# Optimization experiments

Hardware: AMD Instinct MI355X
Metric: run time of the kernel (lower is better)

## Reference

```python
import jax, jax.numpy as jnp
import numpy as np

T, B = 128, 4096
TB = T * B
NUM_ACTIONS, N_WORDS, EMB = 6, 16, 16
IMG_FEAT, LOC_DIM, HID = 16, 4, 128
IN_DIM = IMG_FEAT + LOC_DIM + EMB  # 36
GRID_SIZE = 5.0


def setup_inputs() -> dict:
    key = jax.random.key(0)
    ks = jax.random.split(key, 32)
    p = lambda i, shape, s=0.1: (jax.random.normal(ks[i], shape, dtype=jnp.float32) * s)
    inp = {
        'image': jax.random.uniform(ks[0], (TB, 1, 3, 3), dtype=jnp.float32) * 255.0,
        'location': jax.random.uniform(ks[1], (TB, 2), dtype=jnp.float32) * GRID_SIZE,
        'message': jax.random.randint(ks[2], (TB,), 0, N_WORDS, dtype=jnp.int32),
        'done': (jax.random.uniform(ks[3], (TB,)) < 0.05).astype(jnp.float32),
        'h0': p(4, (B, HID)),
        'c0': p(5, (B, HID)),
        # visual encoder 9->256->256->128->16
        'vw1': p(6, (256, 9)), 'vb1': p(7, (256,)),
        'vw2': p(8, (256, 256)), 'vb2': p(9, (256,)),
        'vw3': p(10, (128, 256)), 'vb3': p(11, (128,)),
        'vw4': p(12, (IMG_FEAT, 128)), 'vb4': p(13, (IMG_FEAT,)),
        # message encoder: embedding + linear
        'emb': p(14, (N_WORDS, EMB)),
        'mw': p(15, (EMB, EMB)), 'mb': p(16, (EMB,)),
        # location encoder 2->4
        'lw': p(17, (LOC_DIM, 2)), 'lb': p(18, (LOC_DIM,)),
        # LSTM (PyTorch layout: gates ordered i,f,g,o)
        'w_ih': p(19, (4 * HID, IN_DIM)), 'w_hh': p(20, (4 * HID, HID)),
        'b_ih': p(21, (4 * HID,)), 'b_hh': p(22, (4 * HID,)),
        # heads
        'aw': p(23, (NUM_ACTIONS, HID), 0.01), 'ab': jnp.zeros((NUM_ACTIONS,), jnp.float32),
        'cw': p(24, (1, HID), 1.0), 'cb': jnp.zeros((1,), jnp.float32),
        'msw': p(25, (N_WORDS, HID), 0.01), 'msb': jnp.zeros((N_WORDS,), jnp.float32),
    }
    return inp


def _encode(image, location, message, vw1, vb1, vw2, vb2, vw3, vb3, vw4, vb4,
            emb, mw, mb, lw, lb):
    img = image.reshape(image.shape[0], -1) / 255.0  # [TB, 9]
    h = jax.nn.relu(img @ vw1.T + vb1)
    h = jax.nn.relu(h @ vw2.T + vb2)
    h = jax.nn.relu(h @ vw3.T + vb3)
    img_feat = jax.nn.relu(h @ vw4.T + vb4)           # [TB, 16]
    loc_feat = (location / GRID_SIZE) @ lw.T + lb     # [TB, 4]
    msg_feat = jax.nn.relu(emb[message] @ mw.T + mb)  # [TB, 16]
    return jnp.concatenate([img_feat, loc_feat, msg_feat], axis=1)  # [TB, 36]


def _lstm_scan(x, done, h0, c0, w_ih, w_hh, b_ih, b_hh):
    # x: [T, B, IN], done: [T, B]
    def step(carry, inp):
        h, c = carry
        xt, dt = inp
        mask = (1.0 - dt)[:, None]
        h = h * mask
        c = c * mask
        gates = xt @ w_ih.T + b_ih + h @ w_hh.T + b_hh  # [B, 4H]
        i, f, g, o = jnp.split(gates, 4, axis=1)
        i = jax.nn.sigmoid(i); f = jax.nn.sigmoid(f)
        g = jnp.tanh(g); o = jax.nn.sigmoid(o)
        c = f * c + i * g
        h = o * jnp.tanh(c)
        return (h, c), h
    (hN, cN), hs = jax.lax.scan(step, (h0, c0), (x, done))
    return hs, hN, cN


def reference(image, location, message, done, h0, c0,
              vw1, vb1, vw2, vb2, vw3, vb3, vw4, vb4,
              emb, mw, mb, lw, lb,
              w_ih, w_hh, b_ih, b_hh,
              aw, ab, cw, cb, msw, msb):
    feat = _encode(image, location, message, vw1, vb1, vw2, vb2, vw3, vb3,
                   vw4, vb4, emb, mw, mb, lw, lb)
    x = feat.reshape(T, B, IN_DIM)
    d = done.reshape(T, B)
    hs, hN, cN = _lstm_scan(x, d, h0, c0, w_ih, w_hh, b_ih, b_hh)
    hidden = hs.reshape(TB, HID)
    action_logits = hidden @ aw.T + ab    # [TB, num_actions]
    message_logits = hidden @ msw.T + msb  # [TB, n_words]
    value = hidden @ cw.T + cb            # [TB, 1]
    return hidden, action_logits, message_logits, value, hN, cN
```

## Files before the change

kernel.cpp:

```cpp
#include <hip/hip_runtime.h>
#include <hip/hip_fp16.h>

typedef _Float16 half8 __attribute__((ext_vector_type(8)));
typedef float f32x4 __attribute__((ext_vector_type(4)));

#define MFMA16(a, b, c) __builtin_amdgcn_mfma_f32_16x16x32_f16((a), (b), (c), 0, 0, 0)
#define DEVI __device__ __forceinline__

static constexpr int T_ = 128, B_ = 4096, HID_ = 128;
static constexpr int TB_ = T_ * B_;

static constexpr size_t W1P = 0;
static constexpr size_t W2P = 8192;
static constexpr size_t W3P = 73728;
static constexpr size_t W4P = 106496;
static constexpr size_t WHL = 108544;
static constexpr size_t MSGT = 305152;
static constexpr size_t HDW = 305408;
static constexpr size_t FEAT = 309504;
static constexpr size_t WS_HALFS = FEAT + (size_t)TB_ * 40;

static constexpr size_t OUT_ACT = (size_t)TB_ * 128;
static constexpr size_t OUT_MSG = OUT_ACT + (size_t)TB_ * 6;
static constexpr size_t OUT_VAL = OUT_MSG + (size_t)TB_ * 16;
static constexpr size_t OUT_HN  = OUT_VAL + (size_t)TB_;
static constexpr size_t OUT_CN  = OUT_HN + (size_t)B_ * 128;

DEVI float sigm_(float x) { return __builtin_amdgcn_rcpf(1.f + __expf(-x)); }
DEVI float tanh_(float x) { return 1.f - 2.f * __builtin_amdgcn_rcpf(1.f + __expf(2.f * x)); }

DEVI void lds_barrier() {
    asm volatile("s_waitcnt lgkmcnt(0)" ::: "memory");
    __builtin_amdgcn_s_barrier();
    asm volatile("" ::: "memory");
}

DEVI void pack_one(const float* __restrict__ src, _Float16* __restrict__ dst,
                   int KT, int srcN, int srcK, int total, int idx) {
    if (idx >= total) return;
    int j = idx & 7, l = (idx >> 3) & 63, rest = idx >> 9;
    int kt = rest % KT, nt = rest / KT;
    int n = nt * 16 + (l & 15);
    int k = kt * 32 + ((l >> 4) << 3) + j;
    float v = (n < srcN && k < srcK) ? src[n * srcK + k] : 0.f;
    dst[idx] = (_Float16)v;
}

__global__ void k_prep(const float* __restrict__ vw1, const float* __restrict__ vw2,
                       const float* __restrict__ vw3, const float* __restrict__ vw4,
                       const float* __restrict__ wih, const float* __restrict__ whh,
                       const float* __restrict__ emb, const float* __restrict__ mw,
                       const float* __restrict__ mb, const float* __restrict__ bih,
                       const float* __restrict__ bhh,
                       const float* __restrict__ aw, const float* __restrict__ ab,
                       const float* __restrict__ cw, const float* __restrict__ cb,
                       const float* __restrict__ msw, const float* __restrict__ msb,
                       _Float16* __restrict__ wsh, float* __restrict__ bcomb) {
    const int blk = blockIdx.x, tid = threadIdx.x;
    if (blk < 768) {
        int idx = blk * 256 + tid;
        int j = idx & 7, l = (idx >> 3) & 63, rest = idx >> 9;
        int kt = rest % 12, nt = rest / 12;
        int n = nt * 16 + (l & 15);
        int k = (kt % 6) * 32 + ((l >> 4) << 3) + j;
        float v;
        if (k < 64) v = (k < 36) ? wih[n * 36 + k] : 0.f;
        else        v = whh[n * 128 + (k - 64)];
        float hi = (float)(_Float16)v;
        wsh[WHL + idx] = (kt < 6) ? (_Float16)hi : (_Float16)(v - hi);
    } else if (blk < 800) {
        pack_one(vw1, wsh + W1P, 1, 256, 9, 8192, (blk - 768) * 256 + tid);
    } else if (blk < 1056) {
        pack_one(vw2, wsh + W2P, 8, 256, 256, 65536, (blk - 800) * 256 + tid);
    } else if (blk < 1184) {
        pack_one(vw3, wsh + W3P, 8, 128, 256, 32768, (blk - 1056) * 256 + tid);
    } else if (blk < 1192) {
        pack_one(vw4, wsh + W4P, 4, 16, 128, 2048, (blk - 1184) * 256 + tid);
    } else if (blk == 1192) {
        int w = tid >> 4, j = tid & 15;
        float a = mb[j];
        for (int e = 0; e < 16; ++e) a += emb[w * 16 + e] * mw[j * 16 + e];
        wsh[MSGT + tid] = (_Float16)fmaxf(a, 0.f);
    } else if (blk < 1195) {
        int i = (blk - 1193) * 256 + tid;
        bcomb[i] = bih[i] + bhh[i];
    } else if (blk < 1211) {
        int idx = (blk - 1195) * 256 + tid;
        int j = idx & 7, l = (idx >> 3) & 63, rest = idx >> 9;
        int kt = rest & 3, nt = rest >> 2;
        int n = nt * 16 + (l & 15);
        int k = kt * 32 + ((l >> 4) << 3) + j;
        float v = (n < 6) ? aw[n * 128 + k]
                : (n < 22) ? msw[(n - 6) * 128 + k]
                : (n == 22) ? cw[k] : 0.f;
        wsh[HDW + idx] = (_Float16)v;
    } else {
        if (tid < 32) {
            float* hb = bcomb + 512;
            hb[tid] = (tid < 6) ? ab[tid] : (tid < 22) ? msb[tid - 6]
                    : (tid == 22) ? cb[0] : 0.f;
        }
    }
}

__global__ __launch_bounds__(256, 2)
void k_encoder(const float* __restrict__ img, const float* __restrict__ loc,
               const int* __restrict__ msg,
               const float* __restrict__ vb1, const float* __restrict__ vb2,
               const float* __restrict__ vb3, const float* __restrict__ vb4,
               const float* __restrict__ lw, const float* __restrict__ lb,
               const _Float16* __restrict__ wsh, _Float16* __restrict__ feat) {
    __shared__ __align__(16) _Float16 sA[64 * 40];
    __shared__ __align__(16) _Float16 sU[64 * 264];
    __shared__ __align__(16) _Float16 sV[64 * 264];
    __shared__ int smsg[64];

    const int tid = threadIdx.x;
    const int lane = tid & 63, wv = tid >> 6;
    const int lq = lane >> 4, lr = lane & 15;
    const int rowbase = blockIdx.x * 64;

    for (int i = tid; i < 576; i += 256) {
        int m = i / 9, k = i - m * 9;
        sA[m * 40 + k] = (_Float16)(img[(size_t)rowbase * 9 + i] * (1.f / 255.f));
    }
    for (int i = tid; i < 64 * 32; i += 256) {
        int m = i >> 5, k = 9 + (i & 31);
        if (k < 40) sA[m * 40 + k] = (_Float16)0.f;
    }
    if (tid < 64) smsg[tid] = msg[rowbase + tid];
    __syncthreads();

    const half8* w1p = (const half8*)(wsh + W1P);
    const half8* w2p = (const half8*)(wsh + W2P);
    const half8* w3p = (const half8*)(wsh + W3P);
    const half8* w4p = (const half8*)(wsh + W4P);

    {
        half8 afr[4];
        #pragma unroll
        for (int mt = 0; mt < 4; ++mt)
            afr[mt] = *(const half8*)&sA[(mt * 16 + lr) * 40 + lq * 8];
        #pragma unroll
        for (int ntl = 0; ntl < 4; ++ntl) {
            const int nt = wv * 4 + ntl;
            half8 bfr = w1p[nt * 64 + lane];
            f32x4 acc[4];
            #pragma unroll
            for (int mt = 0; mt < 4; ++mt) acc[mt] = (f32x4){0.f, 0.f, 0.f, 0.f};
            #pragma unroll
            for (int mt = 0; mt < 4; ++mt) acc[mt] = MFMA16(afr[mt], bfr, acc[mt]);
            const int n = nt * 16 + lr;
            const float bias = vb1[n];
            #pragma unroll
            for (int mt = 0; mt < 4; ++mt)
                #pragma unroll
                for (int r = 0; r < 4; ++r)
                    sU[(mt * 16 + lq * 4 + r) * 264 + n] = (_Float16)fmaxf(acc[mt][r] + bias, 0.f);
        }
    }
    __syncthreads();

    {
        half8 afr[4][8];
        #pragma unroll
        for (int mt = 0; mt < 4; ++mt)
            #pragma unroll
            for (int kt = 0; kt < 8; ++kt)
                afr[mt][kt] = *(const half8*)&sU[(mt * 16 + lr) * 264 + kt * 32 + lq * 8];
        #pragma unroll
        for (int ntl = 0; ntl < 4; ++ntl) {
            const int nt = wv * 4 + ntl;
            half8 bfr[8];
            #pragma unroll
            for (int kt = 0; kt < 8; ++kt) bfr[kt] = w2p[(nt * 8 + kt) * 64 + lane];
            f32x4 acc[4];
            #pragma unroll
            for (int mt = 0; mt < 4; ++mt) acc[mt] = (f32x4){0.f, 0.f, 0.f, 0.f};
            #pragma unroll
            for (int kt = 0; kt < 8; ++kt)
                #pragma unroll
                for (int mt = 0; mt < 4; ++mt)
                    acc[mt] = MFMA16(afr[mt][kt], bfr[kt], acc[mt]);
            const int n = nt * 16 + lr;
            const float bias = vb2[n];
            #pragma unroll
            for (int mt = 0; mt < 4; ++mt)
                #pragma unroll
                for (int r = 0; r < 4; ++r)
                    sV[(mt * 16 + lq * 4 + r) * 264 + n] = (_Float16)fmaxf(acc[mt][r] + bias, 0.f);
        }
    }
    __syncthreads();

    {
        half8 afr[4][8];
        #pragma unroll
        for (int mt = 0; mt < 4; ++mt)
            #pragma unroll
            for (int kt = 0; kt < 8; ++kt)
                afr[mt][kt] = *(const half8*)&sV[(mt * 16 + lr) * 264 + kt * 32 + lq * 8];
        #pragma unroll
        for (int ntl = 0; ntl < 2; ++ntl) {
            const int nt = wv * 2 + ntl;
            half8 bfr[8];
            #pragma unroll
            for (int kt = 0; kt < 8; ++kt) bfr[kt] = w3p[(nt * 8 + kt) * 64 + lane];
            f32x4 acc[4];
            #pragma unroll
            for (int mt = 0; mt < 4; ++mt) acc[mt] = (f32x4){0.f, 0.f, 0.f, 0.f};
            #pragma unroll
            for (int kt = 0; kt < 8; ++kt)
                #pragma unroll
                for (int mt = 0; mt < 4; ++mt)
                    acc[mt] = MFMA16(afr[mt][kt], bfr[kt], acc[mt]);
            const int n = nt * 16 + lr;
            const float bias = vb3[n];
            #pragma unroll
            for (int mt = 0; mt < 4; ++mt)
                #pragma unroll
                for (int r = 0; r < 4; ++r)
                    sU[(mt * 16 + lq * 4 + r) * 264 + n] = (_Float16)fmaxf(acc[mt][r] + bias, 0.f);
        }
    }
    __syncthreads();

    {
        half8 b4[4], a4[4];
        #pragma unroll
        for (int kt = 0; kt < 4; ++kt) {
            b4[kt] = w4p[kt * 64 + lane];
            a4[kt] = *(const half8*)&sU[(wv * 16 + lr) * 264 + kt * 32 + lq * 8];
        }
        f32x4 acc = (f32x4){0.f, 0.f, 0.f, 0.f};
        #pragma unroll
        for (int kt = 0; kt < 4; ++kt) acc = MFMA16(a4[kt], b4[kt], acc);
        const float bias = vb4[lr];
        #pragma unroll
        for (int r = 0; r < 4; ++r)
            sA[(wv * 16 + lq * 4 + r) * 40 + lr] = (_Float16)fmaxf(acc[r] + bias, 0.f);
    }

    {
        int m = tid >> 2, o = tid & 3;
        float x0 = loc[(size_t)(rowbase + m) * 2 + 0] * 0.2f;
        float x1 = loc[(size_t)(rowbase + m) * 2 + 1] * 0.2f;
        sA[m * 40 + 16 + o] = (_Float16)(x0 * lw[o * 2 + 0] + x1 * lw[o * 2 + 1] + lb[o]);
    }
    {
        const _Float16* mst = wsh + MSGT;
        for (int f = tid; f < 1024; f += 256) {
            int m = f >> 4, c = f & 15;
            sA[m * 40 + 20 + c] = mst[smsg[m] * 16 + c];
        }
    }
    {
        int m = tid >> 2, c = 36 + (tid & 3);
        sA[m * 40 + c] = (_Float16)0.f;
    }
    __syncthreads();

    uint4* dst = (uint4*)(feat + (size_t)rowbase * 40);
    const uint4* srcv = (const uint4*)sA;
    for (int i = tid; i < 320; i += 256) dst[i] = srcv[i];
}

__global__ __attribute__((amdgpu_flat_work_group_size(512, 512)))
__attribute__((amdgpu_waves_per_eu(2, 2)))
void k_lstm8(const _Float16* __restrict__ wsh, const float* __restrict__ bcomb,
             const float* __restrict__ done, const float* __restrict__ h0,
             const float* __restrict__ c0, float* __restrict__ hid,
             float* __restrict__ hN, float* __restrict__ cN) {
    __shared__ __align__(16) _Float16 sH[2][16 * 136];
    __shared__ __align__(16) _Float16 sX[2][16 * 72];
    __shared__ __align__(16) float sDm[2][16];

    const int tid = threadIdx.x;
    const int w = tid >> 6, lane = tid & 63;
    const int lq = lane >> 4, lr = lane & 15;
    const int b0 = blockIdx.x * 16;
    const int j = w * 16 + lr;
    const _Float16* feat = wsh + FEAT;
    const half8* wlt = (const half8*)(wsh + WHL);

    half8 wfr[4][12];
    #pragma unroll
    for (int g = 0; g < 4; ++g)
        #pragma unroll
        for (int kt = 0; kt < 12; ++kt)
            wfr[g][kt] = wlt[((8 * g + w) * 12 + kt) * 64 + lane];

    float bias[4];
    #pragma unroll
    for (int g = 0; g < 4; ++g) bias[g] = bcomb[g * 128 + j];

    const half8 hz = {0, 0, 0, 0, 0, 0, 0, 0};

    f32x4 cc, hl;
    #pragma unroll
    for (int r = 0; r < 4; ++r) cc[r] = c0[(size_t)(b0 + lq * 4 + r) * 128 + j];

    for (int i = tid; i < 2048; i += 512) {
        int m = i >> 7, k = i & 127;
        sH[0][m * 136 + k] = (_Float16)h0[(size_t)(b0 + m) * 128 + k];
    }
    for (int i = tid; i < 1024; i += 512) {
        int bb = i >> 9, rem = i & 511;
        int m = rem >> 5, c = 40 + (rem & 31);
        sX[bb][m * 72 + c] = (_Float16)0.f;
    }
    const bool stx = tid < 160;
    const int sm = tid / 10, sc = tid - sm * 10;
    if (stx) *(uint2*)(&sX[0][sm * 72 + sc * 4]) =
        *(const uint2*)(feat + (size_t)(b0 + sm) * 40 + sc * 4);
    if (tid < 16) sDm[0][tid] = 1.f - done[b0 + tid];

    uint2 xrA = {0, 0}, xrB = {0, 0};
    float drA = 0.f, drB = 0.f;
    if (stx) xrA = *(const uint2*)(feat + ((size_t)B_ + b0 + sm) * 40 + sc * 4);
    if (tid < 16) drA = done[(size_t)B_ + b0 + tid];

    const _Float16* fptr = feat + ((size_t)2 * B_ + b0 + sm) * 40 + sc * 4;
    const float* dptr = done + (size_t)2 * B_ + b0 + tid;
    float* hq = hid + (size_t)b0 * 128 + j;

    __syncthreads();

    for (int t = 0; t < T_; ++t) {
        const int p = t & 1;
        const bool pf1 = (t + 1 < T_);
        const bool pf2 = (t + 2 < T_);

        if (stx && pf1) *(uint2*)(&sX[1 - p][sm * 72 + sc * 4]) = xrA;
        if (tid < 16 && pf1) sDm[1 - p][tid] = 1.f - drA;

        if (stx && pf2) xrB = *(const uint2*)fptr;
        if (tid < 16 && pf2) drB = dptr[0];
        fptr += (size_t)B_ * 40;
        dptr += B_;

        if (t > 0) {
            #pragma unroll
            for (int r = 0; r < 4; ++r)
                hq[(size_t)(lq * 4 + r) * 128] = hl[r];
            hq += (size_t)B_ * 128;
        }

        const f32x4 dmv = *(const f32x4*)&sDm[p][lq * 4];
        const float dml = sDm[p][lr];
        const bool keep = (dml != 0.f);

        f32x4 acc[4];
        #pragma unroll
        for (int g = 0; g < 4; ++g)
            acc[g] = (f32x4){bias[g], bias[g], bias[g], bias[g]};

        {
            half8 x0 = *(const half8*)&sX[p][lr * 72 + lq * 8];
            half8 x1 = *(const half8*)&sX[p][lr * 72 + 32 + lq * 8];
            #pragma unroll
            for (int g = 0; g < 4; ++g) acc[g] = MFMA16(x0, wfr[g][0], acc[g]);
            #pragma unroll
            for (int g = 0; g < 4; ++g) acc[g] = MFMA16(x0, wfr[g][6], acc[g]);
            #pragma unroll
            for (int g = 0; g < 4; ++g) acc[g] = MFMA16(x1, wfr[g][1], acc[g]);
            #pragma unroll
            for (int g = 0; g < 4; ++g) acc[g] = MFMA16(x1, wfr[g][7], acc[g]);
        }

        #pragma unroll
        for (int u = 0; u < 4; ++u) {
            half8 av = *(const half8*)&sH[p][lr * 136 + u * 32 + lq * 8];
            av = keep ? av : hz;
            #pragma unroll
            for (int g = 0; g < 4; ++g) acc[g] = MFMA16(av, wfr[g][2 + u], acc[g]);
            #pragma unroll
            for (int g = 0; g < 4; ++g) acc[g] = MFMA16(av, wfr[g][8 + u], acc[g]);
        }

        #pragma unroll
        for (int r = 0; r < 4; ++r) {
            const int m = lq * 4 + r;
            float iv = sigm_(acc[0][r]);
            float fv = sigm_(acc[1][r]);
            float gv = tanh_(acc[2][r]);
            float ov = sigm_(acc[3][r]);
            float cn = fv * (cc[r] * dmv[r]) + iv * gv;
            float hv = ov * tanh_(cn);
            cc[r] = cn;
            hl[r] = hv;
            sH[1 - p][m * 136 + j] = (_Float16)hv;
        }

        lds_barrier();
        xrA = xrB;
        drA = drB;
    }

    #pragma unroll
    for (int r = 0; r < 4; ++r) {
        hq[(size_t)(lq * 4 + r) * 128] = hl[r];
        hN[(size_t)(b0 + lq * 4 + r) * 128 + j] = hl[r];
        cN[(size_t)(b0 + lq * 4 + r) * 128 + j] = cc[r];
    }
}

__global__ __launch_bounds__(256)
void k_heads(const float* __restrict__ hidden, const _Float16* __restrict__ wsh,
             const float* __restrict__ bcomb, float* __restrict__ oact,
             float* __restrict__ omsg, float* __restrict__ oval) {
    __shared__ __align__(16) _Float16 sHd[64 * 136];
    const int tid = threadIdx.x;
    const int w = tid >> 6, lane = tid & 63;
    const int lq = lane >> 4, lr = lane & 15;
    const int rowbase = blockIdx.x * 64;

    {
        const int m = tid >> 2, q = tid & 3;
        const float* src = hidden + (size_t)(rowbase + m) * 128 + q * 32;
        #pragma unroll
        for (int s = 0; s < 4; ++s) {
            f32x4 a = *(const f32x4*)(src + s * 8);
            f32x4 b = *(const f32x4*)(src + s * 8 + 4);
            half8 pk;
            #pragma unroll
            for (int e = 0; e < 4; ++e) pk[e] = (_Float16)a[e];
            #pragma unroll
            for (int e = 0; e < 4; ++e) pk[4 + e] = (_Float16)b[e];
            *(half8*)&sHd[m * 136 + q * 32 + s * 8] = pk;
        }
    }
    __syncthreads();

    half8 av[4];
    #pragma unroll
    for (int kt = 0; kt < 4; ++kt)
        av[kt] = *(const half8*)&sHd[(w * 16 + lr) * 136 + kt * 32 + lq * 8];

    const half8* hwp = (const half8*)(wsh + HDW);
    const float* hb = bcomb + 512;
    #pragma unroll
    for (int nt = 0; nt < 2; ++nt) {
        const float b0 = hb[nt * 16 + lr];
        f32x4 hacc = (f32x4){b0, b0, b0, b0};
        #pragma unroll
        for (int kt = 0; kt < 4; ++kt)
            hacc = MFMA16(av[kt], hwp[(nt * 4 + kt) * 64 + lane], hacc);
        const int o = nt * 16 + lr;
        #pragma unroll
        for (int r = 0; r < 4; ++r) {
            const size_t row = (size_t)rowbase + w * 16 + lq * 4 + r;
            float vv = hacc[r];
            if (o < 6)        oact[row * 6 + o] = vv;
            else if (o < 22)  omsg[row * 16 + (o - 6)] = vv;
            else if (o == 22) oval[row] = vv;
        }
    }
}

extern "C" void kernel_launch(void* const* d_in, const int* in_sizes, int n_in,
                              void* d_out, int out_size, void* d_ws, size_t ws_size,
                              hipStream_t stream) {
    const float* image = (const float*)d_in[0];
    const float* location = (const float*)d_in[1];
    const int*   message = (const int*)d_in[2];
    const float* done = (const float*)d_in[3];
    const float* h0 = (const float*)d_in[4];
    const float* c0 = (const float*)d_in[5];
    const float* vw1 = (const float*)d_in[6];  const float* vb1 = (const float*)d_in[7];
    const float* vw2 = (const float*)d_in[8];  const float* vb2 = (const float*)d_in[9];
    const float* vw3 = (const float*)d_in[10]; const float* vb3 = (const float*)d_in[11];
    const float* vw4 = (const float*)d_in[12]; const float* vb4 = (const float*)d_in[13];
    const float* emb = (const float*)d_in[14];
    const float* mw = (const float*)d_in[15];  const float* mb = (const float*)d_in[16];
    const float* lw = (const float*)d_in[17];  const float* lb = (const float*)d_in[18];
    const float* wih = (const float*)d_in[19]; const float* whh = (const float*)d_in[20];
    const float* bih = (const float*)d_in[21]; const float* bhh = (const float*)d_in[22];
    const float* aw = (const float*)d_in[23];  const float* ab = (const float*)d_in[24];
    const float* cw = (const float*)d_in[25];  const float* cb = (const float*)d_in[26];
    const float* msw = (const float*)d_in[27]; const float* msb = (const float*)d_in[28];

    _Float16* wsh = (_Float16*)d_ws;
    float* bcomb = (float*)((char*)d_ws + WS_HALFS * 2);

    float* out = (float*)d_out;
    float* oh   = out;
    float* oact = out + OUT_ACT;
    float* omsg = out + OUT_MSG;
    float* oval = out + OUT_VAL;
    float* ohN  = out + OUT_HN;
    float* ocN  = out + OUT_CN;

    k_prep<<<1212, 256, 0, stream>>>(vw1, vw2, vw3, vw4, wih, whh, emb, mw, mb,
                                     bih, bhh, aw, ab, cw, cb, msw, msb,
                                     wsh, bcomb);
    k_encoder<<<TB_ / 64, 256, 0, stream>>>(image, location, message, vb1, vb2, vb3, vb4,
                                            lw, lb, wsh, wsh + FEAT);
    k_lstm8<<<B_ / 16, 512, 0, stream>>>(wsh, bcomb, done, h0, c0, oh, ohN, ocN);
    k_heads<<<TB_ / 64, 256, 0, stream>>>(oh, wsh, bcomb, oact, omsg, oval);
}
```

Before: 460.2 us.

## Retile encoder MLP to 128-row blocks with 8 waves and stationary weight fragments

The encoder now processes 128 rows per 512-thread block instead of 64 rows per 256 threads. Each wave keeps its weight fragments for one or two output tiles in registers and loops over all eight row tiles, reading activation fragments from shared memory per row tile. This halves the number of blocks and the total global weight fragment loads per row, at the cost of about doubling shared memory per block (~140KB), which limits residency to one block per CU.

```diff
diff --git a/kernel.cpp b/kernel.cpp
--- a/kernel.cpp
+++ b/kernel.cpp
@@ -103,32 +103,33 @@
     }
 }
 
-__global__ __launch_bounds__(256, 2)
+__global__ __attribute__((amdgpu_flat_work_group_size(512, 512)))
+__attribute__((amdgpu_waves_per_eu(2, 2)))
 void k_encoder(const float* __restrict__ img, const float* __restrict__ loc,
                const int* __restrict__ msg,
                const float* __restrict__ vb1, const float* __restrict__ vb2,
                const float* __restrict__ vb3, const float* __restrict__ vb4,
                const float* __restrict__ lw, const float* __restrict__ lb,
                const _Float16* __restrict__ wsh, _Float16* __restrict__ feat) {
-    __shared__ __align__(16) _Float16 sA[64 * 40];
-    __shared__ __align__(16) _Float16 sU[64 * 264];
-    __shared__ __align__(16) _Float16 sV[64 * 264];
-    __shared__ int smsg[64];
+    __shared__ __align__(16) _Float16 sA[128 * 40];
+    __shared__ __align__(16) _Float16 sU[128 * 264];
+    __shared__ __align__(16) _Float16 sV[128 * 264];
+    __shared__ int smsg[128];
 
     const int tid = threadIdx.x;
-    const int lane = tid & 63, wv = tid >> 6;
+    const int lane = tid & 63, w = tid >> 6;
     const int lq = lane >> 4, lr = lane & 15;
-    const int rowbase = blockIdx.x * 64;
-
-    for (int i = tid; i < 576; i += 256) {
+    const int rowbase = blockIdx.x * 128;
+
+    for (int i = tid; i < 1152; i += 512) {
         int m = i / 9, k = i - m * 9;
         sA[m * 40 + k] = (_Float16)(img[(size_t)rowbase * 9 + i] * (1.f / 255.f));
     }
-    for (int i = tid; i < 64 * 32; i += 256) {
+    for (int i = tid; i < 128 * 32; i += 512) {
         int m = i >> 5, k = 9 + (i & 31);
         if (k < 40) sA[m * 40 + k] = (_Float16)0.f;
     }
-    if (tid < 64) smsg[tid] = msg[rowbase + tid];
+    if (tid < 128) smsg[tid] = msg[rowbase + tid];
     __syncthreads();
 
     const half8* w1p = (const half8*)(wsh + W1P);
@@ -137,108 +138,96 @@
     const half8* w4p = (const half8*)(wsh + W4P);
 
     {
-        half8 afr[4];
-        #pragma unroll
-        for (int mt = 0; mt < 4; ++mt)
-            afr[mt] = *(const half8*)&sA[(mt * 16 + lr) * 40 + lq * 8];
-        #pragma unroll
-        for (int ntl = 0; ntl < 4; ++ntl) {
-            const int nt = wv * 4 + ntl;
-            half8 bfr = w1p[nt * 64 + lane];
-            f32x4 acc[4];
-            #pragma unroll
-            for (int mt = 0; mt < 4; ++mt) acc[mt] = (f32x4){0.f, 0.f, 0.f, 0.f};
-            #pragma unroll
-            for (int mt = 0; mt < 4; ++mt) acc[mt] = MFMA16(afr[mt], bfr, acc[mt]);
-            const int n = nt * 16 + lr;
-            const float bias = vb1[n];
-            #pragma unroll
-            for (int mt = 0; mt < 4; ++mt)
-                #pragma unroll
-                for (int r = 0; r < 4; ++r)
-                    sU[(mt * 16 + lq * 4 + r) * 264 + n] = (_Float16)fmaxf(acc[mt][r] + bias, 0.f);
-        }
-    }
-    __syncthreads();
-
-    {
-        half8 afr[4][8];
-        #pragma unroll
-        for (int mt = 0; mt < 4; ++mt)
+        half8 bfr0 = w1p[(2 * w + 0) * 64 + lane];
+        half8 bfr1 = w1p[(2 * w + 1) * 64 + lane];
+        const float b0 = vb1[(2 * w + 0) * 16 + lr];
+        const float b1 = vb1[(2 * w + 1) * 16 + lr];
+        #pragma unroll
+        for (int mt = 0; mt < 8; ++mt) {
+            half8 afr = *(const half8*)&sA[(mt * 16 + lr) * 40 + lq * 8];
+            f32x4 a0 = (f32x4){0.f, 0.f, 0.f, 0.f};
+            f32x4 a1 = (f32x4){0.f, 0.f, 0.f, 0.f};
+            a0 = MFMA16(afr, bfr0, a0);
+            a1 = MFMA16(afr, bfr1, a1);
+            #pragma unroll
+            for (int r = 0; r < 4; ++r) {
+                sU[(mt * 16 + lq * 4 + r) * 264 + (2 * w + 0) * 16 + lr] =
+                    (_Float16)fmaxf(a0[r] + b0, 0.f);
+                sU[(mt * 16 + lq * 4 + r) * 264 + (2 * w + 1) * 16 + lr] =
+                    (_Float16)fmaxf(a1[r] + b1, 0.f);
+            }
+        }
+    }
+    __syncthreads();
+
+    {
+        half8 bfr[2][8];
+        #pragma unroll
+        for (int n = 0; n < 2; ++n)
             #pragma unroll
             for (int kt = 0; kt < 8; ++kt)
-                afr[mt][kt] = *(const half8*)&sU[(mt * 16 + lr) * 264 + kt * 32 + lq * 8];
-        #pragma unroll
-        for (int ntl = 0; ntl < 4; ++ntl) {
-            const int nt = wv * 4 + ntl;
-            half8 bfr[8];
-            #pragma unroll
-            for (int kt = 0; kt < 8; ++kt) bfr[kt] = w2p[(nt * 8 + kt) * 64 + lane];
-            f32x4 acc[4];
-            #pragma unroll
-            for (int mt = 0; mt < 4; ++mt) acc[mt] = (f32x4){0.f, 0.f, 0.f, 0.f};
+                bfr[n][kt] = w2p[((2 * w + n) * 8 + kt) * 64 + lane];
+        const float b0 = vb2[(2 * w + 0) * 16 + lr];
+        const float b1 = vb2[(2 * w + 1) * 16 + lr];
+        #pragma unroll
+        for (int mt = 0; mt < 8; ++mt) {
+            half8 afr[8];
             #pragma unroll
             for (int kt = 0; kt < 8; ++kt)
-                #pragma unroll
-                for (int mt = 0; mt < 4; ++mt)
-                    acc[mt] = MFMA16(afr[mt][kt], bfr[kt], acc[mt]);
-            const int n = nt * 16 + lr;
-            const float bias = vb2[n];
-            #pragma unroll
-            for (int mt = 0; mt < 4; ++mt)
-                #pragma unroll
-                for (int r = 0; r < 4; ++r)
-                    sV[(mt * 16 + lq * 4 + r) * 264 + n] = (_Float16)fmaxf(acc[mt][r] + bias, 0.f);
-        }
-    }
-    __syncthreads();
-
-    {
-        half8 afr[4][8];
-        #pragma unroll
-        for (int mt = 0; mt < 4; ++mt)
+                afr[kt] = *(const half8*)&sU[(mt * 16 + lr) * 264 + kt * 32 + lq * 8];
+            f32x4 a0 = (f32x4){0.f, 0.f, 0.f, 0.f};
+            f32x4 a1 = (f32x4){0.f, 0.f, 0.f, 0.f};
+            #pragma unroll
+            for (int kt = 0; kt < 8; ++kt) {
+                a0 = MFMA16(afr[kt], bfr[0][kt], a0);
+                a1 = MFMA16(afr[kt], bfr[1][kt], a1);
+            }
+            #pragma unroll
+            for (int r = 0; r < 4; ++r) {
+                sV[(mt * 16 + lq * 4 + r) * 264 + (2 * w + 0) * 16 + lr] =
+                    (_Float16)fmaxf(a0[r] + b0, 0.f);
+                sV[(mt * 16 + lq * 4 + r) * 264 + (2 * w + 1) * 16 + lr] =
+                    (_Float16)fmaxf(a1[r] + b1, 0.f);
+            }
+        }
+    }
+    __syncthreads();
+
+    {
+        half8 bfr[8];
+        #pragma unroll
+        for (int kt = 0; kt < 8; ++kt)
+            bfr[kt] = w3p[(w * 8 + kt) * 64 + lane];
+        const float b0 = vb3[w * 16 + lr];
+        #pragma unroll
+        for (int mt = 0; mt < 8; ++mt) {
+            half8 afr[8];
             #pragma unroll
             for (int kt = 0; kt < 8; ++kt)
-                afr[mt][kt] = *(const half8*)&sV[(mt * 16 + lr) * 264 + kt * 32 + lq * 8];
-        #pragma unroll
-        for (int ntl = 0; ntl < 2; ++ntl) {
-            const int nt = wv * 2 + ntl;
-            half8 bfr[8];
-            #pragma unroll
-            for (int kt = 0; kt < 8; ++kt) bfr[kt] = w3p[(nt * 8 + kt) * 64 + lane];
-            f32x4 acc[4];
-            #pragma unroll
-            for (int mt = 0; mt < 4; ++mt) acc[mt] = (f32x4){0.f, 0.f, 0.f, 0.f};
-            #pragma unroll
-            for (int kt = 0; kt < 8; ++kt)
-                #pragma unroll
-                for (int mt = 0; mt < 4; ++mt)
-                    acc[mt] = MFMA16(afr[mt][kt], bfr[kt], acc[mt]);
-            const int n = nt * 16 + lr;
-            const float bias = vb3[n];
-            #pragma unroll
-            for (int mt = 0; mt < 4; ++mt)
-                #pragma unroll
-                for (int r = 0; r < 4; ++r)
-                    sU[(mt * 16 + lq * 4 + r) * 264 + n] = (_Float16)fmaxf(acc[mt][r] + bias, 0.f);
-        }
-    }
-    __syncthreads();
-
-    {
-        half8 b4[4], a4[4];
+                afr[kt] = *(const half8*)&sV[(mt * 16 + lr) * 264 + kt * 32 + lq * 8];
+            f32x4 a0 = (f32x4){0.f, 0.f, 0.f, 0.f};
+            #pragma unroll
+            for (int kt = 0; kt < 8; ++kt) a0 = MFMA16(afr[kt], bfr[kt], a0);
+            #pragma unroll
+            for (int r = 0; r < 4; ++r)
+                sU[(mt * 16 + lq * 4 + r) * 264 + w * 16 + lr] =
+                    (_Float16)fmaxf(a0[r] + b0, 0.f);
+        }
+    }
+    __syncthreads();
+
+    {
+        f32x4 acc = (f32x4){0.f, 0.f, 0.f, 0.f};
         #pragma unroll
         for (int kt = 0; kt < 4; ++kt) {
-            b4[kt] = w4p[kt * 64 + lane];
-            a4[kt] = *(const half8*)&sU[(wv * 16 + lr) * 264 + kt * 32 + lq * 8];
-        }
-        f32x4 acc = (f32x4){0.f, 0.f, 0.f, 0.f};
-        #pragma unroll
-        for (int kt = 0; kt < 4; ++kt) acc = MFMA16(a4[kt], b4[kt], acc);
+            half8 b4 = w4p[kt * 64 + lane];
+            half8 a4 = *(const half8*)&sU[(w * 16 + lr) * 264 + kt * 32 + lq * 8];
+            acc = MFMA16(a4, b4, acc);
+        }
         const float bias = vb4[lr];
         #pragma unroll
         for (int r = 0; r < 4; ++r)
-            sA[(wv * 16 + lq * 4 + r) * 40 + lr] = (_Float16)fmaxf(acc[r] + bias, 0.f);
+            sA[(w * 16 + lq * 4 + r) * 40 + lr] = (_Float16)fmaxf(acc[r] + bias, 0.f);
     }
 
     {
@@ -249,7 +238,7 @@
     }
     {
         const _Float16* mst = wsh + MSGT;
-        for (int f = tid; f < 1024; f += 256) {
+        for (int f = tid; f < 2048; f += 512) {
             int m = f >> 4, c = f & 15;
             sA[m * 40 + 20 + c] = mst[smsg[m] * 16 + c];
         }
@@ -262,7 +251,7 @@
 
     uint4* dst = (uint4*)(feat + (size_t)rowbase * 40);
     const uint4* srcv = (const uint4*)sA;
-    for (int i = tid; i < 320; i += 256) dst[i] = srcv[i];
+    for (int i = tid; i < 640; i += 512) dst[i] = srcv[i];
 }
 
 __global__ __attribute__((amdgpu_flat_work_group_size(512, 512)))
@@ -494,8 +483,8 @@
     k_prep<<<1212, 256, 0, stream>>>(vw1, vw2, vw3, vw4, wih, whh, emb, mw, mb,
                                      bih, bhh, aw, ab, cw, cb, msw, msb,
                                      wsh, bcomb);
-    k_encoder<<<TB_ / 64, 256, 0, stream>>>(image, location, message, vb1, vb2, vb3, vb4,
-                                            lw, lb, wsh, wsh + FEAT);
+    k_encoder<<<TB_ / 128, 512, 0, stream>>>(image, location, message, vb1, vb2, vb3, vb4,
+                                             lw, lb, wsh, wsh + FEAT);
     k_lstm8<<<B_ / 16, 512, 0, stream>>>(wsh, bcomb, done, h0, c0, oh, ohN, ocN);
     k_heads<<<TB_ / 64, 256, 0, stream>>>(oh, wsh, bcomb, oact, omsg, oval);
 }
```

New measurement: 482.8 us. 1.05x slower.
